# Performance work log

Measured on AMD Instinct MI355X. Metric: run time of the kernel, lower is better.

Reference implementation:

```python
import jax, jax.numpy as jnp
import numpy as np

N, ID, OD, M, S, L = 65536, 16, 8, 1024, 8, 64


def setup_inputs() -> dict:
    key = jax.random.key(0)
    k1, k2, k3, k4, k5, k6 = jax.random.split(key, 6)
    return {
        "x": jax.random.normal(k1, (N, ID), dtype=jnp.float32),
        "inducing_locations": jax.random.uniform(k2, (M, ID), dtype=jnp.float32),
        "inducing_weights": jax.random.normal(k3, (S, OD, M), dtype=jnp.float32),
        "prior_frequency": jax.random.normal(k4, (OD, ID, L), dtype=jnp.float32),
        "prior_phase": jax.random.uniform(k5, (OD, L), dtype=jnp.float32, maxval=2 * np.pi),
        "prior_weights": jax.random.normal(k6, (S, OD, L), dtype=jnp.float32),
    }


def _rbf_matrix(x, z):
    # ExponentiatedQuadratic with amplitude=1, length_scale=1:
    # k(x,z) = exp(-0.5 * ||x - z||^2)
    x2 = jnp.sum(x * x, axis=-1)[:, None]          # [N,1]
    z2 = jnp.sum(z * z, axis=-1)[None, :]          # [1,M]
    sq = jnp.maximum(x2 + z2 - 2.0 * (x @ z.T), 0.0)
    return jnp.exp(-0.5 * sq)                      # [N,M]


def reference(x, inducing_locations, inducing_weights, prior_frequency, prior_phase, prior_weights):
    # ---- prior (random Fourier features) ----
    # spectral_weights for unit RBF: outer_weights = ones((OD,L)), inner_weights = ones((ID,))
    # rescaled_x = x / 1 = x
    # basis_fn_inner_prod: [OD, N, L]
    inner = jnp.einsum('ni,oil->onl', x, prior_frequency)
    basis_fn = jnp.cos(inner + prior_phase[:, None, :])              # [OD,N,L]
    basis_weight = jnp.sqrt(2.0 / prior_frequency.shape[-1]) * prior_weights  # [S,OD,L]
    f_prior = jnp.einsum('onl,sol->son', basis_fn, basis_weight)     # [S,OD,N]

    # ---- data term (kernel matrix + matvec) ----
    K = _rbf_matrix(x, inducing_locations)                           # [N,M]
    f_data = jnp.einsum('nm,som->son', K, inducing_weights)          # [S,OD,N]

    return f_prior + f_data
```

## Files before the change

### kernel.cpp

```cpp
#include <hip/hip_runtime.h>
#include <hip/hip_bf16.h>

#define N_PTS 65536
#define LOG2E 1.4426950408889634f

typedef __attribute__((ext_vector_type(8))) short short8;
typedef __attribute__((ext_vector_type(4))) float float4v;

#if __has_builtin(__builtin_amdgcn_exp2f)
#define EXP2F(x) __builtin_amdgcn_exp2f(x)
#else
#define EXP2F(x) exp2f(x)
#endif

__device__ __forceinline__ short f2b(float f) {
    __hip_bfloat16 h = __float2bfloat16(f);
    return *(short*)&h;
}
__device__ __forceinline__ float b2f(short s) {
    __hip_bfloat16 h = *(__hip_bfloat16*)&s;
    return __bfloat162float(h);
}

__global__ __launch_bounds__(256) void prep_kernel(
    const float* __restrict__ z, const float* __restrict__ W,
    const float* __restrict__ F, const float* __restrict__ pw,
    short* __restrict__ zb, short* __restrict__ FbB,
    short* __restrict__ BWd, short* __restrict__ Wtb,
    float* __restrict__ z2h)
{
    int t = blockIdx.x * 256 + threadIdx.x;
    if (t < 16384) {
        zb[t] = f2b(LOG2E * z[t]);
    } else if (t < 17408) {
        int m = t - 16384;
        const float4v* zp = (const float4v*)(z + (size_t)m * 16);
        float s = 0.f;
        #pragma unroll
        for (int k = 0; k < 4; k++) {
            float4v v = zp[k];
            float a0 = b2f(f2b(v.x)), a1 = b2f(f2b(v.y));
            float a2 = b2f(f2b(v.z)), a3 = b2f(f2b(v.w));
            s += a0 * a0 + a1 * a1 + a2 * a2 + a3 * a3;
        }
        z2h[m] = 0.5f * LOG2E * s;
    } else if (t < 25600) {
        int p = t - 17408;
        int o = p >> 10, l = (p >> 4) & 63, i = p & 15;
        FbB[p] = f2b(F[o * 1024 + i * 64 + l]);
    } else if (t < 58368) {
        int p = t - 25600;
        int so = p >> 9, ol = p & 511, o = ol >> 6;
        float v = ((so & 7) == o) ? 0.17677669529663687f * pw[so * 64 + (ol & 63)] : 0.f;
        BWd[p] = f2b(v);
    } else if (t < 123904) {
        int p = t - 58368;
        Wtb[p] = f2b(W[p]);
    }
}

__global__ __launch_bounds__(256, 4) void fused_kernel(
    const float* __restrict__ x, const float* __restrict__ ph,
    const short* __restrict__ zb, const short* __restrict__ FbB,
    const short* __restrict__ BWd, const short* __restrict__ Wtb,
    const float* __restrict__ z2h, float* __restrict__ out)
{
    __shared__ __align__(16) short tile[2][64 * 136];
    __shared__ float phc[512];
    __shared__ float x2c[64];

    const int tid = threadIdx.x;
    const int lane = tid & 63, w = tid >> 6;
    const int q = lane >> 4, c = lane & 15;
    const int n0 = blockIdx.x * 64;

    for (int i = tid; i < 512; i += 256) phc[i] = ph[i];
    if (tid < 64) {
        float s = 0.f;
        const float4v* xr = (const float4v*)(x + (size_t)(n0 + tid) * 16);
        #pragma unroll
        for (int k = 0; k < 4; k++) {
            float4v v = xr[k];
            float a0 = b2f(f2b(v.x)), a1 = b2f(f2b(v.y));
            float a2 = b2f(f2b(v.z)), a3 = b2f(f2b(v.w));
            s += a0 * a0 + a1 * a1 + a2 * a2 + a3 * a3;
        }
        x2c[tid] = 0.5f * LOG2E * s;
    }

    short8 ax = (short8)0;
    if (q < 2) {
        const float4v* xp = (const float4v*)(x + (size_t)(n0 + 16 * w + c) * 16 + q * 8);
        float4v v0 = xp[0], v1 = xp[1];
        ax[0] = f2b(v0.x); ax[1] = f2b(v0.y); ax[2] = f2b(v0.z); ax[3] = f2b(v0.w);
        ax[4] = f2b(v1.x); ax[5] = f2b(v1.y); ax[6] = f2b(v1.z); ax[7] = f2b(v1.w);
    }

    float4v acc[4];
    #pragma unroll
    for (int i = 0; i < 4; i++) acc[i] = (float4v)(0.f);

    __syncthreads();

    #pragma unroll
    for (int p = 0; p < 4; p++) {
        short* tl = tile[p & 1];
        #pragma unroll
        for (int lt = 0; lt < 8; lt++) {
            short8 bf = (short8)0;
            if (q < 2) bf = *(const short8*)(FbB + ((p * 128 + lt * 16 + c) * 16 + q * 8));
            float phv = phc[p * 128 + lt * 16 + c];
            float4v c0 = {phv, phv, phv, phv};
            float4v d = __builtin_amdgcn_mfma_f32_16x16x32_bf16(ax, bf, c0, 0, 0, 0);
            #pragma unroll
            for (int r = 0; r < 4; r++)
                tl[(16 * w + q * 4 + r) * 136 + lt * 16 + c] = f2b(__cosf(d[r]));
        }
        short8 aw[4];
        #pragma unroll
        for (int ks = 0; ks < 4; ks++)
            aw[ks] = *(const short8*)(BWd + ((16 * w + c) * 512 + p * 128 + ks * 32 + q * 8));
        __syncthreads();
        #pragma unroll
        for (int ks = 0; ks < 4; ks++) {
            #pragma unroll
            for (int nt = 0; nt < 4; nt++) {
                short8 bb = *(const short8*)(tl + (nt * 16 + c) * 136 + ks * 32 + q * 8);
                acc[nt] = __builtin_amdgcn_mfma_f32_16x16x32_bf16(aw[ks], bb, acc[nt], 0, 0, 0);
            }
        }
    }

    float mx2[4];
    #pragma unroll
    for (int r = 0; r < 4; r++) mx2[r] = -x2c[16 * w + q * 4 + r];

    #pragma unroll
    for (int mc = 0; mc < 8; mc++) {
        short* tl = tile[mc & 1];
        int m0 = mc * 128;
        #pragma unroll
        for (int mt = 0; mt < 8; mt++) {
            short8 bz = (short8)0;
            if (q < 2) bz = *(const short8*)(zb + ((m0 + mt * 16 + c) * 16 + q * 8));
            float z2v = z2h[m0 + mt * 16 + c];
            float4v c0;
            #pragma unroll
            for (int r = 0; r < 4; r++) c0[r] = mx2[r] - z2v;
            float4v d = __builtin_amdgcn_mfma_f32_16x16x32_bf16(ax, bz, c0, 0, 0, 0);
            #pragma unroll
            for (int r = 0; r < 4; r++)
                tl[(16 * w + q * 4 + r) * 136 + mt * 16 + c] = f2b(EXP2F(d[r]));
        }
        short8 aw[4];
        #pragma unroll
        for (int ks = 0; ks < 4; ks++)
            aw[ks] = *(const short8*)(Wtb + ((16 * w + c) * 1024 + m0 + ks * 32 + q * 8));
        __syncthreads();
        #pragma unroll
        for (int ks = 0; ks < 4; ks++) {
            #pragma unroll
            for (int nt = 0; nt < 4; nt++) {
                short8 bb = *(const short8*)(tl + (nt * 16 + c) * 136 + ks * 32 + q * 8);
                acc[nt] = __builtin_amdgcn_mfma_f32_16x16x32_bf16(aw[ks], bb, acc[nt], 0, 0, 0);
            }
        }
    }

    #pragma unroll
    for (int nt = 0; nt < 4; nt++) {
        #pragma unroll
        for (int r = 0; r < 4; r++) {
            out[(size_t)(16 * w + q * 4 + r) * N_PTS + n0 + nt * 16 + c] = acc[nt][r];
        }
    }
}

extern "C" void kernel_launch(void* const* d_in, const int* in_sizes, int n_in,
                              void* d_out, int out_size, void* d_ws, size_t ws_size,
                              hipStream_t stream) {
    const float* x  = (const float*)d_in[0];
    const float* z  = (const float*)d_in[1];
    const float* W  = (const float*)d_in[2];
    const float* F  = (const float*)d_in[3];
    const float* ph = (const float*)d_in[4];
    const float* pw = (const float*)d_in[5];
    float* out = (float*)d_out;

    char* ws = (char*)d_ws;
    short* zb  = (short*)(ws);
    short* FbB = (short*)(ws + 32768);
    short* BWd = (short*)(ws + 49152);
    short* Wtb = (short*)(ws + 114688);
    float* z2h = (float*)(ws + 245760);

    prep_kernel<<<484, 256, 0, stream>>>(z, W, F, pw, zb, FbB, BWd, Wtb, z2h);
    fused_kernel<<<1024, 256, 0, stream>>>(x, ph, zb, FbB, BWd, Wtb, z2h, out);
}
```

Before: 122.8 us.

## Split block work across 8 waves and XOR-swizzle the shared tile

New measurement: 157.5 us. 1.28x slower.

```diff
diff --git a/kernel.cpp b/kernel.cpp
--- a/kernel.cpp
+++ b/kernel.cpp
@@ -59,119 +59,129 @@
     }
 }
 
-__global__ __launch_bounds__(256, 4) void fused_kernel(
+__global__ __launch_bounds__(512, 8) void fused_kernel(
     const float* __restrict__ x, const float* __restrict__ ph,
     const short* __restrict__ zb, const short* __restrict__ FbB,
     const short* __restrict__ BWd, const short* __restrict__ Wtb,
     const float* __restrict__ z2h, float* __restrict__ out)
 {
-    __shared__ __align__(16) short tile[2][64 * 136];
-    __shared__ float phc[512];
+    __shared__ __align__(16) short tile[2][64 * 128];
     __shared__ float x2c[64];
 
     const int tid = threadIdx.x;
     const int lane = tid & 63, w = tid >> 6;
     const int q = lane >> 4, c = lane & 15;
+    const int s = w & 3, h = w >> 2;
     const int n0 = blockIdx.x * 64;
 
-    for (int i = tid; i < 512; i += 256) phc[i] = ph[i];
     if (tid < 64) {
-        float s = 0.f;
+        float sum = 0.f;
         const float4v* xr = (const float4v*)(x + (size_t)(n0 + tid) * 16);
         #pragma unroll
         for (int k = 0; k < 4; k++) {
             float4v v = xr[k];
             float a0 = b2f(f2b(v.x)), a1 = b2f(f2b(v.y));
             float a2 = b2f(f2b(v.z)), a3 = b2f(f2b(v.w));
-            s += a0 * a0 + a1 * a1 + a2 * a2 + a3 * a3;
-        }
-        x2c[tid] = 0.5f * LOG2E * s;
+            sum += a0 * a0 + a1 * a1 + a2 * a2 + a3 * a3;
+        }
+        x2c[tid] = 0.5f * LOG2E * sum;
     }
 
     short8 ax = (short8)0;
     if (q < 2) {
-        const float4v* xp = (const float4v*)(x + (size_t)(n0 + 16 * w + c) * 16 + q * 8);
+        const float4v* xp = (const float4v*)(x + (size_t)(n0 + 16 * s + c) * 16 + q * 8);
         float4v v0 = xp[0], v1 = xp[1];
         ax[0] = f2b(v0.x); ax[1] = f2b(v0.y); ax[2] = f2b(v0.z); ax[3] = f2b(v0.w);
         ax[4] = f2b(v1.x); ax[5] = f2b(v1.y); ax[6] = f2b(v1.z); ax[7] = f2b(v1.w);
     }
 
-    float4v acc[4];
-    #pragma unroll
-    for (int i = 0; i < 4; i++) acc[i] = (float4v)(0.f);
+    float4v acc[2];
+    acc[0] = (float4v)(0.f);
+    acc[1] = (float4v)(0.f);
 
     __syncthreads();
 
     #pragma unroll
     for (int p = 0; p < 4; p++) {
         short* tl = tile[p & 1];
-        #pragma unroll
-        for (int lt = 0; lt < 8; lt++) {
+        const int colbase = p * 128 + 64 * h;
+        #pragma unroll
+        for (int lt = 0; lt < 4; lt++) {
+            const int f = colbase + lt * 16 + c;
             short8 bf = (short8)0;
-            if (q < 2) bf = *(const short8*)(FbB + ((p * 128 + lt * 16 + c) * 16 + q * 8));
-            float phv = phc[p * 128 + lt * 16 + c];
+            if (q < 2) bf = *(const short8*)(FbB + (f * 16 + q * 8));
+            float phv = ph[f];
             float4v c0 = {phv, phv, phv, phv};
             float4v d = __builtin_amdgcn_mfma_f32_16x16x32_bf16(ax, bf, c0, 0, 0, 0);
-            #pragma unroll
-            for (int r = 0; r < 4; r++)
-                tl[(16 * w + q * 4 + r) * 136 + lt * 16 + c] = f2b(__cosf(d[r]));
+            const int wb = 8 * h + 2 * lt + (c >> 3);
+            #pragma unroll
+            for (int r = 0; r < 4; r++) {
+                const int row = 16 * s + 4 * q + r;
+                tl[row * 128 + ((wb ^ (row & 7)) * 8) + (c & 7)] = f2b(__cosf(d[r]));
+            }
         }
         short8 aw[4];
         #pragma unroll
         for (int ks = 0; ks < 4; ks++)
-            aw[ks] = *(const short8*)(BWd + ((16 * w + c) * 512 + p * 128 + ks * 32 + q * 8));
+            aw[ks] = *(const short8*)(BWd + ((16 * s + c) * 512 + p * 128 + ks * 32 + q * 8));
         __syncthreads();
         #pragma unroll
         for (int ks = 0; ks < 4; ks++) {
             #pragma unroll
-            for (int nt = 0; nt < 4; nt++) {
-                short8 bb = *(const short8*)(tl + (nt * 16 + c) * 136 + ks * 32 + q * 8);
-                acc[nt] = __builtin_amdgcn_mfma_f32_16x16x32_bf16(aw[ks], bb, acc[nt], 0, 0, 0);
+            for (int ntl = 0; ntl < 2; ntl++) {
+                const int row = (2 * h + ntl) * 16 + c;
+                short8 bb = *(const short8*)(tl + row * 128 + (((ks * 4 + q) ^ (c & 7)) * 8));
+                acc[ntl] = __builtin_amdgcn_mfma_f32_16x16x32_bf16(aw[ks], bb, acc[ntl], 0, 0, 0);
             }
         }
     }
 
     float mx2[4];
     #pragma unroll
-    for (int r = 0; r < 4; r++) mx2[r] = -x2c[16 * w + q * 4 + r];
+    for (int r = 0; r < 4; r++) mx2[r] = -x2c[16 * s + 4 * q + r];
 
     #pragma unroll
     for (int mc = 0; mc < 8; mc++) {
         short* tl = tile[mc & 1];
-        int m0 = mc * 128;
-        #pragma unroll
-        for (int mt = 0; mt < 8; mt++) {
+        const int colbase = mc * 128 + 64 * h;
+        #pragma unroll
+        for (int mt = 0; mt < 4; mt++) {
+            const int m = colbase + mt * 16 + c;
             short8 bz = (short8)0;
-            if (q < 2) bz = *(const short8*)(zb + ((m0 + mt * 16 + c) * 16 + q * 8));
-            float z2v = z2h[m0 + mt * 16 + c];
+            if (q < 2) bz = *(const short8*)(zb + (m * 16 + q * 8));
+            float z2v = z2h[m];
             float4v c0;
             #pragma unroll
             for (int r = 0; r < 4; r++) c0[r] = mx2[r] - z2v;
             float4v d = __builtin_amdgcn_mfma_f32_16x16x32_bf16(ax, bz, c0, 0, 0, 0);
-            #pragma unroll
-            for (int r = 0; r < 4; r++)
-                tl[(16 * w + q * 4 + r) * 136 + mt * 16 + c] = f2b(EXP2F(d[r]));
+            const int wb = 8 * h + 2 * mt + (c >> 3);
+            #pragma unroll
+            for (int r = 0; r < 4; r++) {
+                const int row = 16 * s + 4 * q + r;
+                tl[row * 128 + ((wb ^ (row & 7)) * 8) + (c & 7)] = f2b(EXP2F(d[r]));
+            }
         }
         short8 aw[4];
         #pragma unroll
         for (int ks = 0; ks < 4; ks++)
-            aw[ks] = *(const short8*)(Wtb + ((16 * w + c) * 1024 + m0 + ks * 32 + q * 8));
+            aw[ks] = *(const short8*)(Wtb + ((16 * s + c) * 1024 + mc * 128 + ks * 32 + q * 8));
         __syncthreads();
         #pragma unroll
         for (int ks = 0; ks < 4; ks++) {
             #pragma unroll
-            for (int nt = 0; nt < 4; nt++) {
-                short8 bb = *(const short8*)(tl + (nt * 16 + c) * 136 + ks * 32 + q * 8);
-                acc[nt] = __builtin_amdgcn_mfma_f32_16x16x32_bf16(aw[ks], bb, acc[nt], 0, 0, 0);
-            }
-        }
-    }
-
-    #pragma unroll
-    for (int nt = 0; nt < 4; nt++) {
+            for (int ntl = 0; ntl < 2; ntl++) {
+                const int row = (2 * h + ntl) * 16 + c;
+                short8 bb = *(const short8*)(tl + row * 128 + (((ks * 4 + q) ^ (c & 7)) * 8));
+                acc[ntl] = __builtin_amdgcn_mfma_f32_16x16x32_bf16(aw[ks], bb, acc[ntl], 0, 0, 0);
+            }
+        }
+    }
+
+    #pragma unroll
+    for (int ntl = 0; ntl < 2; ntl++) {
         #pragma unroll
         for (int r = 0; r < 4; r++) {
-            out[(size_t)(16 * w + q * 4 + r) * N_PTS + n0 + nt * 16 + c] = acc[nt][r];
+            out[(size_t)(16 * s + 4 * q + r) * N_PTS + n0 + (2 * h + ntl) * 16 + c] = acc[ntl][r];
         }
     }
 }
@@ -195,5 +205,5 @@
     float* z2h = (float*)(ws + 245760);
 
     prep_kernel<<<484, 256, 0, stream>>>(z, W, F, pw, zb, FbB, BWd, Wtb, z2h);
-    fused_kernel<<<1024, 256, 0, stream>>>(x, ph, zb, FbB, BWd, Wtb, z2h, out);
-}
+    fused_kernel<<<1024, 512, 0, stream>>>(x, ph, zb, FbB, BWd, Wtb, z2h, out);
+}
```

## Prefetch next chunk operands into registers and use hardware cosine in revolutions

Applied to the files above, without the earlier changes.

Result: slower. 136.0 us (+10.8%).

```diff
diff --git a/kernel.cpp b/kernel.cpp
--- a/kernel.cpp
+++ b/kernel.cpp
@@ -3,8 +3,10 @@
 
 #define N_PTS 65536
 #define LOG2E 1.4426950408889634f
+#define INV2PI 0.15915494309189535f
 
 typedef __attribute__((ext_vector_type(8))) short short8;
+typedef __attribute__((ext_vector_type(4))) short short4v;
 typedef __attribute__((ext_vector_type(4))) float float4v;
 
 #if __has_builtin(__builtin_amdgcn_exp2f)
@@ -13,6 +15,12 @@
 #define EXP2F(x) exp2f(x)
 #endif
 
+#if __has_builtin(__builtin_amdgcn_cosf) && __has_builtin(__builtin_amdgcn_fractf)
+#define COS_REV(v) __builtin_amdgcn_cosf(__builtin_amdgcn_fractf(v))
+#else
+#define COS_REV(v) __cosf((v) * 6.283185307179586f)
+#endif
+
 __device__ __forceinline__ short f2b(float f) {
     __hip_bfloat16 h = __float2bfloat16(f);
     return *(short*)&h;
@@ -25,9 +33,10 @@
 __global__ __launch_bounds__(256) void prep_kernel(
     const float* __restrict__ z, const float* __restrict__ W,
     const float* __restrict__ F, const float* __restrict__ pw,
+    const float* __restrict__ ph,
     short* __restrict__ zb, short* __restrict__ FbB,
     short* __restrict__ BWd, short* __restrict__ Wtb,
-    float* __restrict__ z2h)
+    float* __restrict__ z2h, float* __restrict__ phs)
 {
     int t = blockIdx.x * 256 + threadIdx.x;
     if (t < 16384) {
@@ -47,7 +56,7 @@
     } else if (t < 25600) {
         int p = t - 17408;
         int o = p >> 10, l = (p >> 4) & 63, i = p & 15;
-        FbB[p] = f2b(F[o * 1024 + i * 64 + l]);
+        FbB[p] = f2b(INV2PI * F[o * 1024 + i * 64 + l]);
     } else if (t < 58368) {
         int p = t - 25600;
         int so = p >> 9, ol = p & 511, o = ol >> 6;
@@ -56,17 +65,20 @@
     } else if (t < 123904) {
         int p = t - 58368;
         Wtb[p] = f2b(W[p]);
+    } else if (t < 124416) {
+        int p = t - 123904;
+        phs[p] = INV2PI * ph[p];
     }
 }
 
 __global__ __launch_bounds__(256, 4) void fused_kernel(
-    const float* __restrict__ x, const float* __restrict__ ph,
+    const float* __restrict__ x,
     const short* __restrict__ zb, const short* __restrict__ FbB,
     const short* __restrict__ BWd, const short* __restrict__ Wtb,
-    const float* __restrict__ z2h, float* __restrict__ out)
+    const float* __restrict__ z2h, const float* __restrict__ phs,
+    float* __restrict__ out)
 {
-    __shared__ __align__(16) short tile[2][64 * 136];
-    __shared__ float phc[512];
+    __shared__ __align__(16) short tile[2][64 * 132];
     __shared__ float x2c[64];
 
     const int tid = threadIdx.x;
@@ -74,7 +86,6 @@
     const int q = lane >> 4, c = lane & 15;
     const int n0 = blockIdx.x * 64;
 
-    for (int i = tid; i < 512; i += 256) phc[i] = ph[i];
     if (tid < 64) {
         float s = 0.f;
         const float4v* xr = (const float4v*)(x + (size_t)(n0 + tid) * 16);
@@ -102,66 +113,97 @@
 
     __syncthreads();
 
+    float mx2[4];
+    #pragma unroll
+    for (int r = 0; r < 4; r++) mx2[r] = -x2c[16 * w + 4 * q + r];
+
+    short8 pb[8];
+    float  psc[8];
+    #pragma unroll
+    for (int lt = 0; lt < 8; lt++) {
+        int f = lt * 16 + c;
+        pb[lt] = (q < 2) ? *(const short8*)(FbB + (f * 16 + q * 8)) : (short8)0;
+        psc[lt] = phs[f];
+    }
+
     #pragma unroll
     for (int p = 0; p < 4; p++) {
-        short* tl = tile[p & 1];
+        short* buf = tile[p & 1];
         #pragma unroll
         for (int lt = 0; lt < 8; lt++) {
-            short8 bf = (short8)0;
-            if (q < 2) bf = *(const short8*)(FbB + ((p * 128 + lt * 16 + c) * 16 + q * 8));
-            float phv = phc[p * 128 + lt * 16 + c];
-            float4v c0 = {phv, phv, phv, phv};
-            float4v d = __builtin_amdgcn_mfma_f32_16x16x32_bf16(ax, bf, c0, 0, 0, 0);
+            float4v c0 = {psc[lt], psc[lt], psc[lt], psc[lt]};
+            float4v d = __builtin_amdgcn_mfma_f32_16x16x32_bf16(ax, pb[lt], c0, 0, 0, 0);
             #pragma unroll
             for (int r = 0; r < 4; r++)
-                tl[(16 * w + q * 4 + r) * 136 + lt * 16 + c] = f2b(__cosf(d[r]));
+                buf[(16 * w + 4 * q + r) * 132 + lt * 16 + c] = f2b(COS_REV(d[r]));
         }
         short8 aw[4];
         #pragma unroll
         for (int ks = 0; ks < 4; ks++)
             aw[ks] = *(const short8*)(BWd + ((16 * w + c) * 512 + p * 128 + ks * 32 + q * 8));
+        if (p < 3) {
+            #pragma unroll
+            for (int lt = 0; lt < 8; lt++) {
+                int f = (p + 1) * 128 + lt * 16 + c;
+                pb[lt] = (q < 2) ? *(const short8*)(FbB + (f * 16 + q * 8)) : (short8)0;
+                psc[lt] = phs[f];
+            }
+        } else {
+            #pragma unroll
+            for (int lt = 0; lt < 8; lt++) {
+                int m = lt * 16 + c;
+                pb[lt] = (q < 2) ? *(const short8*)(zb + (m * 16 + q * 8)) : (short8)0;
+                psc[lt] = z2h[m];
+            }
+        }
         __syncthreads();
         #pragma unroll
         for (int ks = 0; ks < 4; ks++) {
             #pragma unroll
             for (int nt = 0; nt < 4; nt++) {
-                short8 bb = *(const short8*)(tl + (nt * 16 + c) * 136 + ks * 32 + q * 8);
+                const short* tp = buf + (nt * 16 + c) * 132 + ks * 32 + q * 8;
+                short4v lo = *(const short4v*)tp;
+                short4v hi = *(const short4v*)(tp + 4);
+                short8 bb = __builtin_shufflevector(lo, hi, 0, 1, 2, 3, 4, 5, 6, 7);
                 acc[nt] = __builtin_amdgcn_mfma_f32_16x16x32_bf16(aw[ks], bb, acc[nt], 0, 0, 0);
             }
         }
     }
 
-    float mx2[4];
-    #pragma unroll
-    for (int r = 0; r < 4; r++) mx2[r] = -x2c[16 * w + q * 4 + r];
-
     #pragma unroll
     for (int mc = 0; mc < 8; mc++) {
-        short* tl = tile[mc & 1];
-        int m0 = mc * 128;
+        short* buf = tile[mc & 1];
         #pragma unroll
         for (int mt = 0; mt < 8; mt++) {
-            short8 bz = (short8)0;
-            if (q < 2) bz = *(const short8*)(zb + ((m0 + mt * 16 + c) * 16 + q * 8));
-            float z2v = z2h[m0 + mt * 16 + c];
             float4v c0;
             #pragma unroll
-            for (int r = 0; r < 4; r++) c0[r] = mx2[r] - z2v;
-            float4v d = __builtin_amdgcn_mfma_f32_16x16x32_bf16(ax, bz, c0, 0, 0, 0);
+            for (int r = 0; r < 4; r++) c0[r] = mx2[r] - psc[mt];
+            float4v d = __builtin_amdgcn_mfma_f32_16x16x32_bf16(ax, pb[mt], c0, 0, 0, 0);
             #pragma unroll
             for (int r = 0; r < 4; r++)
-                tl[(16 * w + q * 4 + r) * 136 + mt * 16 + c] = f2b(EXP2F(d[r]));
+                buf[(16 * w + 4 * q + r) * 132 + mt * 16 + c] = f2b(EXP2F(d[r]));
         }
         short8 aw[4];
         #pragma unroll
         for (int ks = 0; ks < 4; ks++)
-            aw[ks] = *(const short8*)(Wtb + ((16 * w + c) * 1024 + m0 + ks * 32 + q * 8));
+            aw[ks] = *(const short8*)(Wtb + ((16 * w + c) * 1024 + mc * 128 + ks * 32 + q * 8));
+        if (mc < 7) {
+            #pragma unroll
+            for (int mt = 0; mt < 8; mt++) {
+                int m = (mc + 1) * 128 + mt * 16 + c;
+                pb[mt] = (q < 2) ? *(const short8*)(zb + (m * 16 + q * 8)) : (short8)0;
+                psc[mt] = z2h[m];
+            }
+        }
         __syncthreads();
         #pragma unroll
         for (int ks = 0; ks < 4; ks++) {
             #pragma unroll
             for (int nt = 0; nt < 4; nt++) {
-                short8 bb = *(const short8*)(tl + (nt * 16 + c) * 136 + ks * 32 + q * 8);
+                const short* tp = buf + (nt * 16 + c) * 132 + ks * 32 + q * 8;
+                short4v lo = *(const short4v*)tp;
+                short4v hi = *(const short4v*)(tp + 4);
+                short8 bb = __builtin_shufflevector(lo, hi, 0, 1, 2, 3, 4, 5, 6, 7);
                 acc[nt] = __builtin_amdgcn_mfma_f32_16x16x32_bf16(aw[ks], bb, acc[nt], 0, 0, 0);
             }
         }
@@ -171,7 +213,7 @@
     for (int nt = 0; nt < 4; nt++) {
         #pragma unroll
         for (int r = 0; r < 4; r++) {
-            out[(size_t)(16 * w + q * 4 + r) * N_PTS + n0 + nt * 16 + c] = acc[nt][r];
+            out[(size_t)(16 * w + 4 * q + r) * N_PTS + n0 + nt * 16 + c] = acc[nt][r];
         }
     }
 }
@@ -193,7 +235,8 @@
     short* BWd = (short*)(ws + 49152);
     short* Wtb = (short*)(ws + 114688);
     float* z2h = (float*)(ws + 245760);
-
-    prep_kernel<<<484, 256, 0, stream>>>(z, W, F, pw, zb, FbB, BWd, Wtb, z2h);
-    fused_kernel<<<1024, 256, 0, stream>>>(x, ph, zb, FbB, BWd, Wtb, z2h, out);
-}
+    float* phs = (float*)(ws + 249856);
+
+    prep_kernel<<<486, 256, 0, stream>>>(z, W, F, pw, ph, zb, FbB, BWd, Wtb, z2h, phs);
+    fused_kernel<<<1024, 256, 0, stream>>>(x, zb, FbB, BWd, Wtb, z2h, phs, out);
+}
```

## Halve rows per block, split column tiles across waves, use revolution-based cosine

Applied to the files above, without the earlier changes.

New measurement: 145.2 us. 1.18x slower.

```diff
diff --git a/kernel.cpp b/kernel.cpp
--- a/kernel.cpp
+++ b/kernel.cpp
@@ -3,8 +3,10 @@
 
 #define N_PTS 65536
 #define LOG2E 1.4426950408889634f
+#define INV2PI 0.15915494309189535f
 
 typedef __attribute__((ext_vector_type(8))) short short8;
+typedef __attribute__((ext_vector_type(4))) short short4v;
 typedef __attribute__((ext_vector_type(4))) float float4v;
 
 #if __has_builtin(__builtin_amdgcn_exp2f)
@@ -13,6 +15,12 @@
 #define EXP2F(x) exp2f(x)
 #endif
 
+#if __has_builtin(__builtin_amdgcn_cosf) && __has_builtin(__builtin_amdgcn_fractf)
+#define COS_REV(v) __builtin_amdgcn_cosf(__builtin_amdgcn_fractf(v))
+#else
+#define COS_REV(v) __cosf((v) * 6.283185307179586f)
+#endif
+
 __device__ __forceinline__ short f2b(float f) {
     __hip_bfloat16 h = __float2bfloat16(f);
     return *(short*)&h;
@@ -25,9 +33,10 @@
 __global__ __launch_bounds__(256) void prep_kernel(
     const float* __restrict__ z, const float* __restrict__ W,
     const float* __restrict__ F, const float* __restrict__ pw,
+    const float* __restrict__ ph,
     short* __restrict__ zb, short* __restrict__ FbB,
     short* __restrict__ BWd, short* __restrict__ Wtb,
-    float* __restrict__ z2h)
+    float* __restrict__ z2h, float* __restrict__ phs)
 {
     int t = blockIdx.x * 256 + threadIdx.x;
     if (t < 16384) {
@@ -47,7 +56,7 @@
     } else if (t < 25600) {
         int p = t - 17408;
         int o = p >> 10, l = (p >> 4) & 63, i = p & 15;
-        FbB[p] = f2b(F[o * 1024 + i * 64 + l]);
+        FbB[p] = f2b(INV2PI * F[o * 1024 + i * 64 + l]);
     } else if (t < 58368) {
         int p = t - 25600;
         int so = p >> 9, ol = p & 511, o = ol >> 6;
@@ -56,26 +65,29 @@
     } else if (t < 123904) {
         int p = t - 58368;
         Wtb[p] = f2b(W[p]);
-    }
-}
-
-__global__ __launch_bounds__(256, 4) void fused_kernel(
-    const float* __restrict__ x, const float* __restrict__ ph,
+    } else if (t < 124416) {
+        int p = t - 123904;
+        phs[p] = INV2PI * ph[p];
+    }
+}
+
+__global__ __launch_bounds__(256, 8) void fused_kernel(
+    const float* __restrict__ x,
     const short* __restrict__ zb, const short* __restrict__ FbB,
     const short* __restrict__ BWd, const short* __restrict__ Wtb,
-    const float* __restrict__ z2h, float* __restrict__ out)
+    const float* __restrict__ z2h, const float* __restrict__ phs,
+    float* __restrict__ out)
 {
-    __shared__ __align__(16) short tile[2][64 * 136];
-    __shared__ float phc[512];
-    __shared__ float x2c[64];
+    __shared__ __align__(16) short tile[32 * 132];
+    __shared__ float x2c[32];
 
     const int tid = threadIdx.x;
     const int lane = tid & 63, w = tid >> 6;
     const int q = lane >> 4, c = lane & 15;
-    const int n0 = blockIdx.x * 64;
-
-    for (int i = tid; i < 512; i += 256) phc[i] = ph[i];
-    if (tid < 64) {
+    const int rw = w & 1, hp = w >> 1;
+    const int n0 = blockIdx.x * 32;
+
+    if (tid < 32) {
         float s = 0.f;
         const float4v* xr = (const float4v*)(x + (size_t)(n0 + tid) * 16);
         #pragma unroll
@@ -90,31 +102,35 @@
 
     short8 ax = (short8)0;
     if (q < 2) {
-        const float4v* xp = (const float4v*)(x + (size_t)(n0 + 16 * w + c) * 16 + q * 8);
+        const float4v* xp = (const float4v*)(x + (size_t)(n0 + 16 * rw + c) * 16 + q * 8);
         float4v v0 = xp[0], v1 = xp[1];
         ax[0] = f2b(v0.x); ax[1] = f2b(v0.y); ax[2] = f2b(v0.z); ax[3] = f2b(v0.w);
         ax[4] = f2b(v1.x); ax[5] = f2b(v1.y); ax[6] = f2b(v1.z); ax[7] = f2b(v1.w);
     }
 
-    float4v acc[4];
-    #pragma unroll
-    for (int i = 0; i < 4; i++) acc[i] = (float4v)(0.f);
+    float4v acc[2];
+    acc[0] = (float4v)(0.f);
+    acc[1] = (float4v)(0.f);
 
     __syncthreads();
 
+    float mx2[4];
+    #pragma unroll
+    for (int r = 0; r < 4; r++) mx2[r] = -x2c[16 * rw + 4 * q + r];
+
     #pragma unroll
     for (int p = 0; p < 4; p++) {
-        short* tl = tile[p & 1];
-        #pragma unroll
-        for (int lt = 0; lt < 8; lt++) {
+        #pragma unroll
+        for (int lt = 0; lt < 4; lt++) {
+            const int f = p * 128 + hp * 64 + lt * 16 + c;
             short8 bf = (short8)0;
-            if (q < 2) bf = *(const short8*)(FbB + ((p * 128 + lt * 16 + c) * 16 + q * 8));
-            float phv = phc[p * 128 + lt * 16 + c];
+            if (q < 2) bf = *(const short8*)(FbB + (f * 16 + q * 8));
+            float phv = phs[f];
             float4v c0 = {phv, phv, phv, phv};
             float4v d = __builtin_amdgcn_mfma_f32_16x16x32_bf16(ax, bf, c0, 0, 0, 0);
             #pragma unroll
             for (int r = 0; r < 4; r++)
-                tl[(16 * w + q * 4 + r) * 136 + lt * 16 + c] = f2b(__cosf(d[r]));
+                tile[(16 * rw + 4 * q + r) * 132 + hp * 64 + lt * 16 + c] = f2b(COS_REV(d[r]));
         }
         short8 aw[4];
         #pragma unroll
@@ -124,54 +140,57 @@
         #pragma unroll
         for (int ks = 0; ks < 4; ks++) {
             #pragma unroll
-            for (int nt = 0; nt < 4; nt++) {
-                short8 bb = *(const short8*)(tl + (nt * 16 + c) * 136 + ks * 32 + q * 8);
+            for (int nt = 0; nt < 2; nt++) {
+                const short* tp = tile + (nt * 16 + c) * 132 + ks * 32 + q * 8;
+                short4v lo = *(const short4v*)tp;
+                short4v hi = *(const short4v*)(tp + 4);
+                short8 bb = __builtin_shufflevector(lo, hi, 0, 1, 2, 3, 4, 5, 6, 7);
                 acc[nt] = __builtin_amdgcn_mfma_f32_16x16x32_bf16(aw[ks], bb, acc[nt], 0, 0, 0);
             }
         }
-    }
-
-    float mx2[4];
-    #pragma unroll
-    for (int r = 0; r < 4; r++) mx2[r] = -x2c[16 * w + q * 4 + r];
+        __syncthreads();
+    }
 
     #pragma unroll
     for (int mc = 0; mc < 8; mc++) {
-        short* tl = tile[mc & 1];
-        int m0 = mc * 128;
-        #pragma unroll
-        for (int mt = 0; mt < 8; mt++) {
+        #pragma unroll
+        for (int mt = 0; mt < 4; mt++) {
+            const int m = mc * 128 + hp * 64 + mt * 16 + c;
             short8 bz = (short8)0;
-            if (q < 2) bz = *(const short8*)(zb + ((m0 + mt * 16 + c) * 16 + q * 8));
-            float z2v = z2h[m0 + mt * 16 + c];
+            if (q < 2) bz = *(const short8*)(zb + (m * 16 + q * 8));
+            float z2v = z2h[m];
             float4v c0;
             #pragma unroll
             for (int r = 0; r < 4; r++) c0[r] = mx2[r] - z2v;
             float4v d = __builtin_amdgcn_mfma_f32_16x16x32_bf16(ax, bz, c0, 0, 0, 0);
             #pragma unroll
             for (int r = 0; r < 4; r++)
-                tl[(16 * w + q * 4 + r) * 136 + mt * 16 + c] = f2b(EXP2F(d[r]));
+                tile[(16 * rw + 4 * q + r) * 132 + hp * 64 + mt * 16 + c] = f2b(EXP2F(d[r]));
         }
         short8 aw[4];
         #pragma unroll
         for (int ks = 0; ks < 4; ks++)
-            aw[ks] = *(const short8*)(Wtb + ((16 * w + c) * 1024 + m0 + ks * 32 + q * 8));
+            aw[ks] = *(const short8*)(Wtb + ((16 * w + c) * 1024 + mc * 128 + ks * 32 + q * 8));
         __syncthreads();
         #pragma unroll
         for (int ks = 0; ks < 4; ks++) {
             #pragma unroll
-            for (int nt = 0; nt < 4; nt++) {
-                short8 bb = *(const short8*)(tl + (nt * 16 + c) * 136 + ks * 32 + q * 8);
+            for (int nt = 0; nt < 2; nt++) {
+                const short* tp = tile + (nt * 16 + c) * 132 + ks * 32 + q * 8;
+                short4v lo = *(const short4v*)tp;
+                short4v hi = *(const short4v*)(tp + 4);
+                short8 bb = __builtin_shufflevector(lo, hi, 0, 1, 2, 3, 4, 5, 6, 7);
                 acc[nt] = __builtin_amdgcn_mfma_f32_16x16x32_bf16(aw[ks], bb, acc[nt], 0, 0, 0);
             }
         }
-    }
-
-    #pragma unroll
-    for (int nt = 0; nt < 4; nt++) {
+        __syncthreads();
+    }
+
+    #pragma unroll
+    for (int nt = 0; nt < 2; nt++) {
         #pragma unroll
         for (int r = 0; r < 4; r++) {
-            out[(size_t)(16 * w + q * 4 + r) * N_PTS + n0 + nt * 16 + c] = acc[nt][r];
+            out[(size_t)(16 * w + 4 * q + r) * N_PTS + n0 + nt * 16 + c] = acc[nt][r];
         }
     }
 }
@@ -193,7 +212,8 @@
     short* BWd = (short*)(ws + 49152);
     short* Wtb = (short*)(ws + 114688);
     float* z2h = (float*)(ws + 245760);
-
-    prep_kernel<<<484, 256, 0, stream>>>(z, W, F, pw, zb, FbB, BWd, Wtb, z2h);
-    fused_kernel<<<1024, 256, 0, stream>>>(x, ph, zb, FbB, BWd, Wtb, z2h, out);
-}
+    float* phs = (float*)(ws + 249856);
+
+    prep_kernel<<<486, 256, 0, stream>>>(z, W, F, pw, ph, zb, FbB, BWd, Wtb, z2h, phs);
+    fused_kernel<<<2048, 256, 0, stream>>>(x, zb, FbB, BWd, Wtb, z2h, phs, out);
+}
```
